# Performance work log

Hardware: AMD Instinct MI355X
Metric: run time of the kernel (lower is better)

Reference implementation:

```python
import jax, jax.numpy as jnp
import numpy as np

NUM_CHARS = 26  # hardcoded in original module


def setup_inputs() -> dict:
    key = jax.random.key(0)
    ks = jax.random.split(key, 8)
    B, T, H = 2048, 1024, NUM_CHARS
    s = 1.0 / np.sqrt(H)
    return {
        "x": jax.random.randint(ks[0], (B, T), 0, NUM_CHARS, dtype=jnp.int64),
        "E": jax.random.normal(ks[1], (NUM_CHARS, H), dtype=jnp.float32),            # embedding table
        "W_ih": jax.random.uniform(ks[2], (4 * H, H), jnp.float32, -s, s),           # LSTM input weights (i,f,g,o)
        "W_hh": jax.random.uniform(ks[3], (4 * H, H), jnp.float32, -s, s),           # LSTM hidden weights
        "b_ih": jax.random.uniform(ks[4], (4 * H,), jnp.float32, -s, s),
        "b_hh": jax.random.uniform(ks[5], (4 * H,), jnp.float32, -s, s),
        "W_lin": jax.random.uniform(ks[6], (NUM_CHARS, H), jnp.float32, -s, s),      # final Linear weight
        "b_lin": jax.random.uniform(ks[7], (NUM_CHARS,), jnp.float32, -s, s),
    }


def reference(x, E, W_ih, W_hh, b_ih, b_hh, W_lin, b_lin):
    # Embedding lookup: [B,T] -> [B,T,H]
    emb = E[x]
    B, T, H = emb.shape
    # Precompute input projections for all timesteps: [B,T,4H]
    x_proj = jnp.einsum('bth,gh->btg', emb, W_ih) + b_ih

    def step(carry, xt):  # xt: [B,4H]
        h, c = carry
        gates = xt + h @ W_hh.T + b_hh  # [B,4H], torch gate order i,f,g,o
        i, f, g, o = jnp.split(gates, 4, axis=-1)
        i = jax.nn.sigmoid(i)
        f = jax.nn.sigmoid(f)
        g = jnp.tanh(g)
        o = jax.nn.sigmoid(o)
        c = f * c + i * g
        h = o * jnp.tanh(c)
        return (h, c), None

    h0 = jnp.zeros((B, H), emb.dtype)
    (hT, _), _ = jax.lax.scan(step, (h0, h0), jnp.swapaxes(x_proj, 0, 1))
    # h_n has shape [num_layers=1, B, H]; .squeeze(1) is a no-op for B>1
    out = hT @ W_lin.T + b_lin  # [B,26]
    return out[None]  # [1,B,26]
```

## Files before the change

### kernel.cpp

```cpp
#include <hip/hip_runtime.h>

#define LOG2E 1.442695040888963f

typedef float f32x2 __attribute__((ext_vector_type(2)));

static __device__ __forceinline__ void pkfma(f32x2& acc, f32x2 a, f32x2 b) {
    asm("v_pk_fma_f32 %0, %1, %2, %0" : "+v"(acc) : "v"(a), "v"(b));
}
static __device__ __forceinline__ void pkmul(f32x2& d, f32x2 a, f32x2 b) {
    asm("v_pk_mul_f32 %0, %1, %2" : "=v"(d) : "v"(a), "v"(b));
}

__launch_bounds__(64, 2)
__global__ void lstm_char_kernel(const int* __restrict__ x,
                                 const float* __restrict__ E,
                                 const float* __restrict__ W_ih,
                                 const float* __restrict__ W_hh,
                                 const float* __restrict__ b_ih,
                                 const float* __restrict__ b_hh,
                                 const float* __restrict__ W_lin,
                                 const float* __restrict__ b_lin,
                                 float* __restrict__ out,
                                 int T)
{
    constexpr int H = 26;

    __shared__ __align__(16) f32x2 P[26][64];
    __shared__ __align__(8) unsigned short chars[1032];
    __shared__ __align__(16) float hbuf[64];

    const int b = blockIdx.x;
    const int l = threadIdx.x;
    const int j = l & 31;
    const bool lo = (l < 32);
    const int rr = (j < 26) ? j : 0;
    const int r0 = lo ? rr : 26 + rr;
    const int r1 = lo ? 52 + rr : 78 + rr;

    for (int t = l; t < T; t += 64)
        chars[t] = (unsigned short)(x[(size_t)b * T + t] * 512);
    if (l < 8) chars[1024 + l] = 0;
    hbuf[l] = 0.0f;

    const float m0 = -LOG2E;
    const float m1 = lo ? (-2.0f * LOG2E) : (-LOG2E);
    const float s1 = lo ? (-4.0f * LOG2E) : 1.0f;
    const float d1 = lo ? ( 2.0f * LOG2E) : 0.0f;

    f32x2 wh0p[13], wh1p[13];
    #pragma unroll
    for (int k = 0; k < 13; ++k) {
        wh0p[k] = f32x2{W_hh[r0 * H + 2 * k] * m0, W_hh[r0 * H + 2 * k + 1] * m0};
        wh1p[k] = f32x2{W_hh[r1 * H + 2 * k] * m1, W_hh[r1 * H + 2 * k + 1] * m1};
    }

    {
        float wi0[H], wi1[H];
        #pragma unroll
        for (int k = 0; k < H; ++k) {
            wi0[k] = W_ih[r0 * H + k];
            wi1[k] = W_ih[r1 * H + k];
        }
        const float bias0 = b_ih[r0] + b_hh[r0];
        const float bias1 = b_ih[r1] + b_hh[r1];
        for (int ch = 0; ch < 26; ++ch) {
            float a0 = bias0, a1 = bias1;
            #pragma unroll
            for (int k = 0; k < H; ++k) {
                float e = E[ch * H + k];
                a0 = fmaf(wi0[k], e, a0);
                a1 = fmaf(wi1[k], e, a1);
            }
            P[ch][l] = f32x2{a0 * m0, a1 * m1};
        }
    }
    __syncthreads();

    {
        unsigned hsh = (blockIdx.x * 2654435761u) >> 29;
        float dch = (float)(l + 1);
        for (unsigned i = 0; i < hsh; ++i) {
            asm volatile("v_rcp_f32 %0, %0\n\t"
                         "v_rcp_f32 %0, %0\n\t"
                         "v_rcp_f32 %0, %0\n\t"
                         "v_rcp_f32 %0, %0" : "+v"(dch));
        }
        asm volatile("" :: "v"(dch));
    }

    const int hidx = (l - 32) & 63;
    const char* Pb = (const char*)&P[0][0];
    const int lane8 = l << 3;

    int poffn = chars[1];
    f32x2 pa = *(const f32x2*)(Pb + (int)chars[0] + lane8);
    float C = 0.0f;

    #pragma unroll 2
    for (int t = 0; t < T; ++t) {
        f32x2 hp[13];
        #pragma unroll
        for (int q = 0; q < 13; ++q) hp[q] = ((const f32x2*)hbuf)[q];

        f32x2 pn = *(const f32x2*)(Pb + poffn + lane8);
        int poff2 = chars[t + 2];

        f32x2 A0, A1, B0, B1;
        pkmul(A0, hp[0], wh0p[0]);
        pkmul(A1, hp[1], wh0p[1]);
        pkmul(B0, hp[0], wh1p[0]);
        pkmul(B1, hp[1], wh1p[1]);
        #pragma unroll
        for (int k = 2; k < 12; k += 2) {
            pkfma(A0, hp[k],     wh0p[k]);
            pkfma(A1, hp[k + 1], wh0p[k + 1]);
            pkfma(B0, hp[k],     wh1p[k]);
            pkfma(B1, hp[k + 1], wh1p[k + 1]);
        }
        pkfma(A0, hp[12], wh0p[12]);
        pkfma(B0, hp[12], wh1p[12]);
        f32x2 sa = A0 + A1;
        f32x2 sb = B0 + B1;
        const float a0s = sa.x + sa.y + pa.x;
        const float a1s = sb.x + sb.y + pa.y;

        float y0 = __builtin_amdgcn_rcpf(1.0f + __builtin_amdgcn_exp2f(a0s));
        float y1 = fmaf(__builtin_amdgcn_rcpf(1.0f + __builtin_amdgcn_exp2f(a1s)),
                        s1, d1);
        float y1_2 = y1 + y1;

        float pr = y0 * y1;
        auto sw = __builtin_amdgcn_permlane32_swap(__float_as_int(y0),
                                                   __float_as_int(pr),
                                                   false, false);
        float rcv = __int_as_float(sw[0]);

        C = fmaf(y0, C, rcv);
        float rc = __builtin_amdgcn_rcpf(1.0f + __builtin_amdgcn_exp2f(C));
        float hv = fmaf(rc, y1_2, -y1);
        hbuf[hidx] = hv;

        pa = pn; poffn = poff2;
    }

    __syncthreads();

    if (l < H) {
        float acc = b_lin[l];
        #pragma unroll
        for (int k = 0; k < H; ++k)
            acc = fmaf(W_lin[l * H + k], hbuf[k], acc);
        out[(size_t)b * H + l] = acc;
    }
}

extern "C" void kernel_launch(void* const* d_in, const int* in_sizes, int n_in,
                              void* d_out, int out_size, void* d_ws, size_t ws_size,
                              hipStream_t stream) {
    const int*   x     = (const int*)d_in[0];
    const float* E     = (const float*)d_in[1];
    const float* W_ih  = (const float*)d_in[2];
    const float* W_hh  = (const float*)d_in[3];
    const float* b_ih  = (const float*)d_in[4];
    const float* b_hh  = (const float*)d_in[5];
    const float* W_lin = (const float*)d_in[6];
    const float* b_lin = (const float*)d_in[7];
    float* out = (float*)d_out;

    const int T = 1024;
    const int B = in_sizes[0] / T;

    lstm_char_kernel<<<B, 64, 0, stream>>>(x, E, W_ih, W_hh, b_ih, b_hh,
                                           W_lin, b_lin, out, T);
}
```

Before: 276.3 us.

## Broadcast hidden state via readlane instead of LDS round-trip each timestep

```diff
diff --git a/kernel.cpp b/kernel.cpp
--- a/kernel.cpp
+++ b/kernel.cpp
@@ -3,13 +3,6 @@
 #define LOG2E 1.442695040888963f
 
 typedef float f32x2 __attribute__((ext_vector_type(2)));
-
-static __device__ __forceinline__ void pkfma(f32x2& acc, f32x2 a, f32x2 b) {
-    asm("v_pk_fma_f32 %0, %1, %2, %0" : "+v"(acc) : "v"(a), "v"(b));
-}
-static __device__ __forceinline__ void pkmul(f32x2& d, f32x2 a, f32x2 b) {
-    asm("v_pk_mul_f32 %0, %1, %2" : "=v"(d) : "v"(a), "v"(b));
-}
 
 __launch_bounds__(64, 2)
 __global__ void lstm_char_kernel(const int* __restrict__ x,
@@ -27,7 +20,6 @@
 
     __shared__ __align__(16) f32x2 P[26][64];
     __shared__ __align__(8) unsigned short chars[1032];
-    __shared__ __align__(16) float hbuf[64];
 
     const int b = blockIdx.x;
     const int l = threadIdx.x;
@@ -40,18 +32,17 @@
     for (int t = l; t < T; t += 64)
         chars[t] = (unsigned short)(x[(size_t)b * T + t] * 512);
     if (l < 8) chars[1024 + l] = 0;
-    hbuf[l] = 0.0f;
 
     const float m0 = -LOG2E;
     const float m1 = lo ? (-2.0f * LOG2E) : (-LOG2E);
     const float s1 = lo ? (-4.0f * LOG2E) : 1.0f;
     const float d1 = lo ? ( 2.0f * LOG2E) : 0.0f;
 
-    f32x2 wh0p[13], wh1p[13];
+    float wh0[H], wh1[H];
     #pragma unroll
-    for (int k = 0; k < 13; ++k) {
-        wh0p[k] = f32x2{W_hh[r0 * H + 2 * k] * m0, W_hh[r0 * H + 2 * k + 1] * m0};
-        wh1p[k] = f32x2{W_hh[r1 * H + 2 * k] * m1, W_hh[r1 * H + 2 * k + 1] * m1};
+    for (int k = 0; k < H; ++k) {
+        wh0[k] = W_hh[r0 * H + k] * m0;
+        wh1[k] = W_hh[r1 * H + k] * m1;
     }
 
     {
@@ -76,21 +67,12 @@
     }
     __syncthreads();
 
-    {
-        unsigned hsh = (blockIdx.x * 2654435761u) >> 29;
-        float dch = (float)(l + 1);
-        for (unsigned i = 0; i < hsh; ++i) {
-            asm volatile("v_rcp_f32 %0, %0\n\t"
-                         "v_rcp_f32 %0, %0\n\t"
-                         "v_rcp_f32 %0, %0\n\t"
-                         "v_rcp_f32 %0, %0" : "+v"(dch));
-        }
-        asm volatile("" :: "v"(dch));
-    }
-
-    const int hidx = (l - 32) & 63;
     const char* Pb = (const char*)&P[0][0];
     const int lane8 = l << 3;
+
+    float hs[H];
+    #pragma unroll
+    for (int k = 0; k < H; ++k) hs[k] = 0.0f;
 
     int poffn = chars[1];
     f32x2 pa = *(const f32x2*)(Pb + (int)chars[0] + lane8);
@@ -98,31 +80,19 @@
 
     #pragma unroll 2
     for (int t = 0; t < T; ++t) {
-        f32x2 hp[13];
-        #pragma unroll
-        for (int q = 0; q < 13; ++q) hp[q] = ((const f32x2*)hbuf)[q];
-
         f32x2 pn = *(const f32x2*)(Pb + poffn + lane8);
         int poff2 = chars[t + 2];
 
-        f32x2 A0, A1, B0, B1;
-        pkmul(A0, hp[0], wh0p[0]);
-        pkmul(A1, hp[1], wh0p[1]);
-        pkmul(B0, hp[0], wh1p[0]);
-        pkmul(B1, hp[1], wh1p[1]);
+        float u0 = pa.x, u1 = 0.0f, u2 = pa.y, u3 = 0.0f;
         #pragma unroll
-        for (int k = 2; k < 12; k += 2) {
-            pkfma(A0, hp[k],     wh0p[k]);
-            pkfma(A1, hp[k + 1], wh0p[k + 1]);
-            pkfma(B0, hp[k],     wh1p[k]);
-            pkfma(B1, hp[k + 1], wh1p[k + 1]);
+        for (int k = 0; k < H; k += 2) {
+            u0 = fmaf(wh0[k],     hs[k],     u0);
+            u1 = fmaf(wh0[k + 1], hs[k + 1], u1);
+            u2 = fmaf(wh1[k],     hs[k],     u2);
+            u3 = fmaf(wh1[k + 1], hs[k + 1], u3);
         }
-        pkfma(A0, hp[12], wh0p[12]);
-        pkfma(B0, hp[12], wh1p[12]);
-        f32x2 sa = A0 + A1;
-        f32x2 sb = B0 + B1;
-        const float a0s = sa.x + sa.y + pa.x;
-        const float a1s = sb.x + sb.y + pa.y;
+        const float a0s = u0 + u1;
+        const float a1s = u2 + u3;
 
         float y0 = __builtin_amdgcn_rcpf(1.0f + __builtin_amdgcn_exp2f(a0s));
         float y1 = fmaf(__builtin_amdgcn_rcpf(1.0f + __builtin_amdgcn_exp2f(a1s)),
@@ -138,18 +108,20 @@
         C = fmaf(y0, C, rcv);
         float rc = __builtin_amdgcn_rcpf(1.0f + __builtin_amdgcn_exp2f(C));
         float hv = fmaf(rc, y1_2, -y1);
-        hbuf[hidx] = hv;
+
+        const int hb = __float_as_int(hv);
+        #pragma unroll
+        for (int k = 0; k < H; ++k)
+            hs[k] = __int_as_float(__builtin_amdgcn_readlane(hb, 32 + k));
 
         pa = pn; poffn = poff2;
     }
-
-    __syncthreads();
 
     if (l < H) {
         float acc = b_lin[l];
         #pragma unroll
         for (int k = 0; k < H; ++k)
-            acc = fmaf(W_lin[l * H + k], hbuf[k], acc);
+            acc = fmaf(W_lin[l * H + k], hs[k], acc);
         out[(size_t)b * H + l] = acc;
     }
 }
```

After: 342.9 us. 1.24x slower.
